# Performance work log

Measured on AMD Instinct MI355X. Metric: run time of the kernel, lower is better.

Reference implementation:

```python
import jax, jax.numpy as jnp
import numpy as np

B, N, L = 1, 128, 256
D_MSA, D_HID, D_PAIR = 256, 32, 128
EPS = 1e-5


def setup_inputs() -> dict:
    key = jax.random.key(0)
    ks = jax.random.split(key, 8)
    msa = jax.random.normal(ks[0], (B, N, L, D_MSA), dtype=jnp.float32)
    pair = jax.random.normal(ks[1], (B, L, L, D_PAIR), dtype=jnp.float32)
    symmids = jax.random.randint(ks[2], (1,), 0, 1, dtype=jnp.int64)
    symmsub = jax.random.randint(ks[3], (1,), 0, 1, dtype=jnp.int64)
    # learned params (lecun-normal-ish scale = 1/sqrt(fan_in))
    ln_gamma = jnp.ones((D_MSA,), jnp.float32)
    ln_beta = jnp.zeros((D_MSA,), jnp.float32)
    w_left = jax.random.normal(ks[4], (D_MSA, D_HID), jnp.float32) / np.sqrt(D_MSA)
    b_left = jnp.zeros((D_HID,), jnp.float32)
    w_right = jax.random.normal(ks[5], (D_MSA, D_HID), jnp.float32) / np.sqrt(D_MSA)
    b_right = jnp.zeros((D_HID,), jnp.float32)
    w_out = jax.random.normal(ks[6], (D_HID * D_HID, D_PAIR), jnp.float32) / np.sqrt(D_HID * D_HID)
    b_out = jnp.zeros((D_PAIR,), jnp.float32)
    return {
        "msa": msa, "pair": pair, "symmids": symmids, "symmsub": symmsub,
        "ln_gamma": ln_gamma, "ln_beta": ln_beta,
        "w_left": w_left, "b_left": b_left,
        "w_right": w_right, "b_right": b_right,
        "w_out": w_out, "b_out": b_out,
    }


def reference(msa, pair, symmids, symmsub, ln_gamma, ln_beta,
              w_left, b_left, w_right, b_right, w_out, b_out):
    b, n, l, _ = msa.shape
    # LayerNorm over d_msa (biased variance, matching torch)
    mu = jnp.mean(msa, axis=-1, keepdims=True)
    var = jnp.mean(jnp.square(msa - mu), axis=-1, keepdims=True)
    x = (msa - mu) * jax.lax.rsqrt(var + EPS) * ln_gamma + ln_beta
    left = x @ w_left + b_left                       # [b, n, l, d_h]
    right = (x @ w_right + b_right) / float(n)       # [b, n, l, d_h]
    # outer product, reduced over MSA (s) dim -> [b, l, m, d_h, d_h]
    out = jnp.einsum('bsli,bsmj->blmij', left, right).reshape(b, l, l, -1)
    out = out @ w_out + b_out                        # [b, l, l, d_pair]
    return pair + out
```

## Files before the change

kernel.cpp:

```cpp
#include <hip/hip_runtime.h>


typedef float v4f __attribute__((ext_vector_type(4)));
typedef short v8s __attribute__((ext_vector_type(8)));

static __device__ inline unsigned short f2bf(float x) {
    unsigned int u = __builtin_bit_cast(unsigned int, x);
    return (unsigned short)((u + 0x7fffu + ((u >> 16) & 1u)) >> 16);
}

__global__ __launch_bounds__(256) void k_prep(const float* __restrict__ w_out,
                                              const float* __restrict__ wl,
                                              const float* __restrict__ wr,
                                              unsigned short* __restrict__ w3,
                                              unsigned short* __restrict__ wTg) {
    const int b = blockIdx.x, t = threadIdx.x;
    unsigned short tmp[8];
    if (b < 64) {
        int tgt = b * 2048 + t * 8;
        int lane6 = (tgt >> 3) & 63, quad = lane6 >> 4, l15 = lane6 & 15;
        int w = (tgt >> 9) & 3, tt = (tgt >> 11) & 1;
        int inner = (tgt >> 12) & 1, ck = tgt >> 13;
        int p = w * 32 + tt * 16 + l15;
        for (int e = 0; e < 8; ++e) {
            int kp = ck * 64 + inner * 32 + quad * 8 + e;
            int j1 = (kp >> 9) & 1, qd = (kp >> 7) & 3, lp = (kp >> 3) & 15;
            int i1 = (kp >> 2) & 1, r = kp & 3;
            int ii = i1 * 16 + qd * 4 + r, jj = j1 * 16 + lp;
            tmp[e] = f2bf(w_out[(ii * 32 + jj) * 128 + p]);
        }
        *(uint4*)&w3[tgt] = *(const uint4*)tmp;
    } else {
        int tgt = (b - 64) * 2048 + t * 8;
        int c = tgt >> 8, d0 = tgt & 255;
        const float* src = (c < 32) ? wl : wr;
        int cc = c & 31;
        for (int e = 0; e < 8; ++e) tmp[e] = f2bf(src[(d0 + e) * 32 + cc]);
        *(uint4*)&wTg[tgt] = *(const uint4*)tmp;
    }
}

__global__ __launch_bounds__(256) void k_lnproj(
    const float* __restrict__ msa, const float* __restrict__ gamma, const float* __restrict__ beta,
    const unsigned short* __restrict__ wTg, const float* __restrict__ bl, const float* __restrict__ br,
    unsigned short* __restrict__ leftT, unsigned short* __restrict__ rightT) {
    __shared__ unsigned short xb[32 * 264];
    __shared__ unsigned short wlds[64 * 264];
    __shared__ unsigned short outT[64 * 40];

    const int t = threadIdx.x, lane = t & 63, w = t >> 6;
    const int l = blockIdx.x, s0 = blockIdx.y * 32;
    const int quad = lane >> 4, l15 = lane & 15;

    for (int it = 0; it < 8; ++it) {
        int idx = it * 2048 + t * 8;
        *(uint4*)&wlds[(idx >> 8) * 264 + (idx & 255)] = *(const uint4*)&wTg[idx];
    }

    float4 g4 = *(const float4*)&gamma[lane * 4];
    float4 be4 = *(const float4*)&beta[lane * 4];
    float4 vr[8]; float s1[8], s2[8];
    for (int r = 0; r < 8; ++r) {
        const float* row = msa + (size_t)((s0 + w * 8 + r) * 256 + l) * 256;
        vr[r] = *(const float4*)&row[lane * 4];
    }
    for (int r = 0; r < 8; ++r) {
        float4 v = vr[r];
        s1[r] = v.x + v.y + v.z + v.w;
        s2[r] = v.x * v.x + v.y * v.y + v.z * v.z + v.w * v.w;
    }
    for (int o = 32; o > 0; o >>= 1)
        for (int r = 0; r < 8; ++r) { s1[r] += __shfl_xor(s1[r], o); s2[r] += __shfl_xor(s2[r], o); }
    for (int r = 0; r < 8; ++r) {
        float mu = s1[r] * (1.f / 256);
        float rs = rsqrtf(s2[r] * (1.f / 256) - mu * mu + 1e-5f);
        float4 v = vr[r];
        ushort4 xs;
        xs.x = f2bf((v.x - mu) * rs * g4.x + be4.x);
        xs.y = f2bf((v.y - mu) * rs * g4.y + be4.y);
        xs.z = f2bf((v.z - mu) * rs * g4.z + be4.z);
        xs.w = f2bf((v.w - mu) * rs * g4.w + be4.w);
        *(ushort4*)&xb[(w * 8 + r) * 264 + lane * 4] = xs;
    }
    __syncthreads();

    const int mt = w >> 1, ntb = (w & 1) * 2;
    v4f acc[2] = {};
    const int frow = (mt * 16 + l15) * 264;
    for (int ks = 0; ks < 8; ++ks) {
        int k = ks * 32 + quad * 8;
        v8s a = *(const v8s*)&xb[frow + k];
        v8s b0 = *(const v8s*)&wlds[(ntb * 16 + l15) * 264 + k];
        v8s b1 = *(const v8s*)&wlds[((ntb + 1) * 16 + l15) * 264 + k];
        acc[0] = __builtin_amdgcn_mfma_f32_16x16x32_bf16(a, b0, acc[0], 0, 0, 0);
        acc[1] = __builtin_amdgcn_mfma_f32_16x16x32_bf16(a, b1, acc[1], 0, 0, 0);
    }

    for (int tn = 0; tn < 2; ++tn) {
        int c = (ntb + tn) * 16 + l15;
        float bias = c < 32 ? bl[c] : br[c - 32];
        float scale = c < 32 ? 1.f : (1.f / 128);
        for (int r = 0; r < 4; ++r)
            outT[c * 40 + mt * 16 + quad * 4 + r] = f2bf((acc[tn][r] + bias) * scale);
    }
    __syncthreads();

    {
        int c = t >> 2, q = t & 3;
        uint4 vv = *(const uint4*)&outT[c * 40 + q * 8];
        int kh = s0 >> 6;
        int g = ((s0 & 32) >> 3) + q;
        int g2 = g ^ (c & 7);
        unsigned short* dst = (c < 32) ? (leftT + l * 4096 + c * 128)
                                       : (rightT + l * 4096 + (c - 32) * 128);
        *(uint4*)&dst[kh * 64 + g2 * 8] = vv;
    }
}

__global__ __launch_bounds__(256, 4) void k_outer(
    const unsigned short* __restrict__ leftT, const unsigned short* __restrict__ rightT,
    const unsigned short* __restrict__ w2g, const float* __restrict__ bout,
    const float* __restrict__ pairIn, float* __restrict__ out) {
    __shared__ alignas(16) unsigned short smem[16384];
    unsigned short* Ah = smem;
    unsigned short* Bh = smem + 8192;
    unsigned short* Obuf = smem;

    const int t = threadIdx.x, lane = t & 63, w = t >> 6;
    const int l0 = blockIdx.x * 4, m0 = blockIdx.y * 4;
    const int wm = w & 1, wn = w >> 1;
    const int quad = lane >> 4, l15 = lane & 15;

    const unsigned short* Asrc = leftT + l0 * 4096;
    const unsigned short* Bsrc = rightT + m0 * 4096;

    v4f acc[4][4] = {};
    for (int kh = 0; kh < 2; ++kh) {
        __syncthreads();
        for (int it = 0; it < 4; ++it) {
            int el = (it * 256 + t) * 8;
            int m = el >> 6, off = el & 63;
            *(uint4*)&Ah[el] = *(const uint4*)&Asrc[m * 128 + kh * 64 + off];
            *(uint4*)&Bh[el] = *(const uint4*)&Bsrc[m * 128 + kh * 64 + off];
        }
        __syncthreads();
        for (int ks = 0; ks < 2; ++ks) {
            int g = ks * 4 + quad;
            v8s a[4], bb[4];
            for (int i = 0; i < 4; ++i)
                a[i] = *(const v8s*)&Ah[(wm * 64 + i * 16 + l15) * 64 + ((g ^ (l15 & 7)) << 3)];
            for (int j = 0; j < 4; ++j)
                bb[j] = *(const v8s*)&Bh[(wn * 64 + j * 16 + l15) * 64 + ((g ^ (l15 & 7)) << 3)];
            for (int i = 0; i < 4; ++i)
                for (int j = 0; j < 4; ++j)
                    acc[i][j] = __builtin_amdgcn_mfma_f32_16x16x32_bf16(a[i], bb[j], acc[i][j], 0, 0, 0);
        }
    }
    __syncthreads();

    for (int a2 = 0; a2 < 2; ++a2)
        for (int b2 = 0; b2 < 2; ++b2) {
            int pr = (wm * 2 + a2) * 4 + wn * 2 + b2;
            for (int j1 = 0; j1 < 2; ++j1) {
                unsigned short tmp8[8];
                for (int i1 = 0; i1 < 2; ++i1)
                    for (int r = 0; r < 4; ++r)
                        tmp8[i1 * 4 + r] = f2bf(acc[a2 * 2 + i1][b2 * 2 + j1][r]);
                int pg = (j1 * 64 + lane) ^ (pr & 7) ^ ((pr & 8) << 3);
                *(uint4*)&Obuf[pr * 1024 + pg * 8] = *(const uint4*)tmp8;
            }
        }
    __syncthreads();

    v4f acc2[2] = {};
    {
        const unsigned short* wsrc = w2g + w * 512 + lane * 8;
        v8s f0 = *(const v8s*)&wsrc[0];
        v8s f1 = *(const v8s*)&wsrc[2048];
        v8s f2 = *(const v8s*)&wsrc[4096];
        v8s f3 = *(const v8s*)&wsrc[6144];
#pragma unroll
        for (int ck = 0; ck < 16; ++ck) {
            v8s c0 = f0, c1 = f1, c2 = f2, c3 = f3;
            if (ck < 15) {
                const unsigned short* nx = wsrc + (ck + 1) * 8192;
                f0 = *(const v8s*)&nx[0];
                f1 = *(const v8s*)&nx[2048];
                f2 = *(const v8s*)&nx[4096];
                f3 = *(const v8s*)&nx[6144];
            }
            {
                int g = ck * 8 + quad;
                v8s a = *(const v8s*)&Obuf[l15 * 1024 + ((g ^ (l15 & 7) ^ ((l15 & 8) << 3)) << 3)];
                acc2[0] = __builtin_amdgcn_mfma_f32_16x16x32_bf16(a, c0, acc2[0], 0, 0, 0);
                acc2[1] = __builtin_amdgcn_mfma_f32_16x16x32_bf16(a, c1, acc2[1], 0, 0, 0);
            }
            {
                int g = ck * 8 + 4 + quad;
                v8s a = *(const v8s*)&Obuf[l15 * 1024 + ((g ^ (l15 & 7) ^ ((l15 & 8) << 3)) << 3)];
                acc2[0] = __builtin_amdgcn_mfma_f32_16x16x32_bf16(a, c2, acc2[0], 0, 0, 0);
                acc2[1] = __builtin_amdgcn_mfma_f32_16x16x32_bf16(a, c3, acc2[1], 0, 0, 0);
            }
        }
    }

    for (int tt = 0; tt < 2; ++tt) {
        int p = (w * 2 + tt) * 16 + l15;
        float bo = bout[p];
        for (int r = 0; r < 4; ++r) {
            int pr = quad * 4 + r;
            int dl = pr >> 2, dm = pr & 3;
            size_t idx = (size_t)((l0 + dl) * 256 + (m0 + dm)) * 128 + p;
            out[idx] = pairIn[idx] + bo + acc2[tt][r];
        }
    }
}

extern "C" void kernel_launch(void* const* d_in, const int* in_sizes, int n_in,
                              void* d_out, int out_size, void* d_ws, size_t ws_size,
                              hipStream_t stream) {
    const float* msa   = (const float*)d_in[0];
    const float* pairI = (const float*)d_in[1];
    const float* gamma = (const float*)d_in[4];
    const float* beta  = (const float*)d_in[5];
    const float* wl    = (const float*)d_in[6];
    const float* bl    = (const float*)d_in[7];
    const float* wr    = (const float*)d_in[8];
    const float* br    = (const float*)d_in[9];
    const float* wout  = (const float*)d_in[10];
    const float* bout  = (const float*)d_in[11];
    float* out = (float*)d_out;

    unsigned short* leftT  = (unsigned short*)d_ws;
    unsigned short* rightT = leftT + 256 * 32 * 128;
    unsigned short* w3     = rightT + 256 * 32 * 128;
    unsigned short* wTg    = w3 + 131072;

    k_prep<<<dim3(72), 256, 0, stream>>>(wout, wl, wr, w3, wTg);
    k_lnproj<<<dim3(256, 4), 256, 0, stream>>>(msa, gamma, beta, wTg, bl, br, leftT, rightT);
    k_outer<<<dim3(64, 64), 256, 0, stream>>>(leftT, rightT, w3, bout, pairI, out);
}
```

Baseline: 181.7 us.

## Store projections in MFMA fragment order and load operands directly from global

The projection kernel now writes left/right activations in a layout that matches MFMA fragment order per lane. The outer-product kernel can then read A/B operands straight from global memory (L2-resident) instead of staging them through LDS with barriers. The pair input is also prefetched at kernel start so its latency overlaps the compute. The occupancy hint drops from 4 to 3 blocks per CU, and the LDS footprint shrinks to the output buffer only. This trades LDS staging and syncs for more global/L2 traffic and register pressure.

After: 185.2 us. No clear change (+1.9%).

```diff
diff --git a/kernel.cpp b/kernel.cpp
--- a/kernel.cpp
+++ b/kernel.cpp
@@ -108,55 +108,56 @@
     {
         int c = t >> 2, q = t & 3;
         uint4 vv = *(const uint4*)&outT[c * 40 + q * 8];
-        int kh = s0 >> 6;
-        int g = ((s0 & 32) >> 3) + q;
-        int g2 = g ^ (c & 7);
-        unsigned short* dst = (c < 32) ? (leftT + l * 4096 + c * 128)
-                                       : (rightT + l * 4096 + (c - 32) * 128);
-        *(uint4*)&dst[kh * 64 + g2 * 8] = vv;
-    }
-}
-
-__global__ __launch_bounds__(256, 4) void k_outer(
+        int cc = c & 31;
+        unsigned short* base = (c < 32) ? leftT : rightT;
+        unsigned short* dst = base + l * 4096 + blockIdx.y * 1024
+                            + (cc >> 4) * 512 + q * 128 + (cc & 15) * 8;
+        *(uint4*)dst = vv;
+    }
+}
+
+__global__ __launch_bounds__(256, 3) void k_outer(
     const unsigned short* __restrict__ leftT, const unsigned short* __restrict__ rightT,
     const unsigned short* __restrict__ w2g, const float* __restrict__ bout,
     const float* __restrict__ pairIn, float* __restrict__ out) {
-    __shared__ alignas(16) unsigned short smem[16384];
-    unsigned short* Ah = smem;
-    unsigned short* Bh = smem + 8192;
-    unsigned short* Obuf = smem;
+    __shared__ alignas(16) unsigned short Obuf[16384];
 
     const int t = threadIdx.x, lane = t & 63, w = t >> 6;
     const int l0 = blockIdx.x * 4, m0 = blockIdx.y * 4;
     const int wm = w & 1, wn = w >> 1;
     const int quad = lane >> 4, l15 = lane & 15;
 
+    float pf[8];
+#pragma unroll
+    for (int tt = 0; tt < 2; ++tt)
+#pragma unroll
+        for (int r = 0; r < 4; ++r) {
+            int pr = quad * 4 + r;
+            int dl = pr >> 2, dm = pr & 3;
+            int p = (w * 2 + tt) * 16 + l15;
+            size_t idx = (size_t)((l0 + dl) * 256 + (m0 + dm)) * 128 + p;
+            pf[tt * 4 + r] = pairIn[idx];
+        }
+
     const unsigned short* Asrc = leftT + l0 * 4096;
     const unsigned short* Bsrc = rightT + m0 * 4096;
 
     v4f acc[4][4] = {};
-    for (int kh = 0; kh < 2; ++kh) {
-        __syncthreads();
-        for (int it = 0; it < 4; ++it) {
-            int el = (it * 256 + t) * 8;
-            int m = el >> 6, off = el & 63;
-            *(uint4*)&Ah[el] = *(const uint4*)&Asrc[m * 128 + kh * 64 + off];
-            *(uint4*)&Bh[el] = *(const uint4*)&Bsrc[m * 128 + kh * 64 + off];
-        }
-        __syncthreads();
-        for (int ks = 0; ks < 2; ++ks) {
-            int g = ks * 4 + quad;
-            v8s a[4], bb[4];
-            for (int i = 0; i < 4; ++i)
-                a[i] = *(const v8s*)&Ah[(wm * 64 + i * 16 + l15) * 64 + ((g ^ (l15 & 7)) << 3)];
+#pragma unroll
+    for (int kk = 0; kk < 4; ++kk) {
+        v8s a[4], bb[4];
+#pragma unroll
+        for (int i = 0; i < 4; ++i)
+            a[i] = *(const v8s*)&Asrc[(wm * 2 + (i >> 1)) * 4096 + kk * 1024 + (i & 1) * 512 + lane * 8];
+#pragma unroll
+        for (int j = 0; j < 4; ++j)
+            bb[j] = *(const v8s*)&Bsrc[(wn * 2 + (j >> 1)) * 4096 + kk * 1024 + (j & 1) * 512 + lane * 8];
+#pragma unroll
+        for (int i = 0; i < 4; ++i)
+#pragma unroll
             for (int j = 0; j < 4; ++j)
-                bb[j] = *(const v8s*)&Bh[(wn * 64 + j * 16 + l15) * 64 + ((g ^ (l15 & 7)) << 3)];
-            for (int i = 0; i < 4; ++i)
-                for (int j = 0; j < 4; ++j)
-                    acc[i][j] = __builtin_amdgcn_mfma_f32_16x16x32_bf16(a[i], bb[j], acc[i][j], 0, 0, 0);
-        }
-    }
-    __syncthreads();
+                acc[i][j] = __builtin_amdgcn_mfma_f32_16x16x32_bf16(a[i], bb[j], acc[i][j], 0, 0, 0);
+    }
 
     for (int a2 = 0; a2 < 2; ++a2)
         for (int b2 = 0; b2 < 2; ++b2) {
@@ -204,14 +205,16 @@
         }
     }
 
+#pragma unroll
     for (int tt = 0; tt < 2; ++tt) {
         int p = (w * 2 + tt) * 16 + l15;
         float bo = bout[p];
+#pragma unroll
         for (int r = 0; r < 4; ++r) {
             int pr = quad * 4 + r;
             int dl = pr >> 2, dm = pr & 3;
             size_t idx = (size_t)((l0 + dl) * 256 + (m0 + dm)) * 128 + p;
-            out[idx] = pairIn[idx] + bo + acc2[tt][r];
+            out[idx] = pf[tt * 4 + r] + bo + acc2[tt][r];
         }
     }
 }
```
